# Kernel optimization log

Hardware: AMD Instinct MI355X
Metric: run time of the kernel (lower is better)

## Reference

```python
import jax, jax.numpy as jnp
import numpy as np

TOP_K = 2  # num_expert in the torch module


def setup_inputs() -> dict:
    key = jax.random.key(0)
    ks = jax.random.split(key, 8)
    B, C, H, W, E, Dh = 8, 512, 32, 32, 8, 1024
    inputs = jax.random.normal(ks[0], (B, C, H, W), dtype=jnp.float32)
    k = jax.random.uniform(ks[1], (B, 1, 1, 1), dtype=jnp.float32)
    # gate: global-avg-pool + Linear(C -> E)
    Wg = jax.random.normal(ks[2], (C, E), dtype=jnp.float32) / np.sqrt(C)
    bg = jnp.zeros((E,), dtype=jnp.float32)
    # experts: per-expert 2-layer channel MLP (1x1-conv style), modulated by k
    W1 = jax.random.normal(ks[3], (E, C, Dh), dtype=jnp.float32) / np.sqrt(C)
    b1 = jnp.zeros((E, Dh), dtype=jnp.float32)
    W2 = jax.random.normal(ks[4], (E, Dh, C), dtype=jnp.float32) / np.sqrt(Dh)
    b2 = jnp.zeros((E, C), dtype=jnp.float32)
    return {"inputs": inputs, "k": k, "Wg": Wg, "bg": bg,
            "W1": W1, "b1": b1, "W2": W2, "b2": b2}


def reference(inputs, k, Wg, bg, W1, b1, W2, b2):
    B = inputs.shape[0]
    # --- gate: softmax in fp32, cast back (matches F.softmax(dtype=torch.float)) ---
    logits = jnp.mean(inputs, axis=(2, 3)) @ Wg + bg            # [B, E]
    weights = jax.nn.softmax(logits.astype(jnp.float32), axis=1).astype(inputs.dtype)
    topk_w, topk_idx = jax.lax.top_k(weights, TOP_K)            # [B, K]
    # --- scatter top-k gate weights into dense [B, E] mask (training path) ---
    exp_w = jnp.zeros_like(weights).at[jnp.arange(B)[:, None], topk_idx].set(topk_w)
    # --- run ALL experts densely (training-mode math), masked combine ---
    h = jnp.einsum('bchw,ecd->bedhw', inputs, W1) + b1[None, :, :, None, None]
    h = jax.nn.gelu(h, approximate=False)                        # [B,E,Dh,H,W]
    y = jnp.einsum('bedhw,edc->bechw', h, W2) + b2[None, :, :, None, None]
    y = y * k[:, None]                                           # per-sample scalar mod
    out = inputs + jnp.einsum('bechw,be->bchw', y, exp_w)        # residual + weighted sum
    return out
```

## Files before the change

### kernel.cpp

```cpp
#include <hip/hip_runtime.h>
#include <hip/hip_bf16.h>
#include <math.h>


typedef __bf16 bf16_t;
typedef __attribute__((ext_vector_type(8))) __bf16 bf16x8;
typedef __attribute__((ext_vector_type(4))) __bf16 bf16x4;
typedef __attribute__((ext_vector_type(4))) float f32x4;

#define GLDS(g, l) __builtin_amdgcn_global_load_lds(                      \
    (const __attribute__((address_space(1))) void*)(const void*)(g),       \
    (__attribute__((address_space(3))) void*)(void*)(l), 16, 0, 0)

__device__ __forceinline__ int xcd_swz(int bid, int grid) {
    return (bid & 7) * (grid >> 3) + (bid >> 3);
}

__device__ __forceinline__ float gelu_fast(float x) {
    float z = x * 0.70710678118654752f;
    float az = fabsf(z);
    float t = 1.0f / (1.0f + 0.3275911f * az);
    float p = ((((1.061405429f * t - 1.453152027f) * t + 1.421413741f) * t
                - 0.284496736f) * t + 0.254829592f) * t;
    float e = __expf(-az * az);
    float er = copysignf(1.0f - p * e, z);
    return 0.5f * x * (1.0f + er);
}

__global__ __launch_bounds__(256) void transpose_cvt_all(
    const float* __restrict__ x, const float* __restrict__ W1,
    const float* __restrict__ W2, bf16_t* __restrict__ xT,
    bf16_t* __restrict__ W1t, bf16_t* __restrict__ W2t, float* __restrict__ pp) {
    int id = blockIdx.x;
    const float* src; bf16_t* dst; int Rows, Cols, csh; bool dm = false;
    if (id < 1024)      { src = x;  dst = xT;  Rows = 512;  Cols = 1024; csh = 4; dm = true; }
    else if (id < 2048) { id -= 1024; src = W1; dst = W1t; Rows = 512;  Cols = 1024; csh = 4; }
    else                { id -= 2048; src = W2; dst = W2t; Rows = 1024; Cols = 512; csh = 3; }
    const int bz = id >> 7, t = id & 127;
    const int ct = t & ((1 << csh) - 1), rt = t >> csh;
    const int r0 = rt * 64, c0 = ct * 64;
    __shared__ float tile[64][65];
    const int tid = threadIdx.x;
    const int lrw = tid >> 4, lcol = (tid & 15) * 4;
    const float* sb = src + (size_t)bz * Rows * Cols + c0;
    #pragma unroll
    for (int p = 0; p < 4; ++p) {
        const int row = p * 16 + lrw;
        float4 v = *(const float4*)(sb + (size_t)(r0 + row) * Cols + lcol);
        tile[row][lcol + 0] = v.x; tile[row][lcol + 1] = v.y;
        tile[row][lcol + 2] = v.z; tile[row][lcol + 3] = v.w;
    }
    __syncthreads();
    if (dm) {
        const int row = tid >> 2, q = tid & 3;
        float s = 0.f;
        #pragma unroll
        for (int j = 0; j < 16; ++j) s += tile[row][q * 16 + j];
        s += __shfl_down(s, 2, 4);
        s += __shfl_down(s, 1, 4);
        if (q == 0) pp[(bz * 16 + ct) * 512 + r0 + row] = s;
    }
    bf16_t* db = dst + (size_t)bz * Rows * Cols + r0;
    #pragma unroll
    for (int q = 0; q < 2; ++q) {
        const int idq = q * 256 + tid;
        const int orow = idq >> 3, seg = idq & 7;
        bf16_t ov[8];
        #pragma unroll
        for (int j = 0; j < 8; ++j) ov[j] = (bf16_t)tile[seg * 8 + j][orow];
        *(bf16x8*)(db + (size_t)(c0 + orow) * Rows + seg * 8) = *(bf16x8*)ov;
    }
}

__global__ void gate_kernel(const float* __restrict__ pp, const float* __restrict__ Wg,
                            const float* __restrict__ bg, const float* __restrict__ kmod,
                            int* __restrict__ tidx, float* __restrict__ scale) {
    const int b = blockIdx.x;
    const int tid = threadIdx.x;
    const int lane = tid & 63, wave = tid >> 6;
    float a[8] = {0.f, 0.f, 0.f, 0.f, 0.f, 0.f, 0.f, 0.f};
    #pragma unroll
    for (int rep = 0; rep < 2; ++rep) {
        const int c = rep * 256 + tid;
        float m = 0.f;
        #pragma unroll
        for (int ht = 0; ht < 16; ++ht) m += pp[(b * 16 + ht) * 512 + c];
        #pragma unroll
        for (int e = 0; e < 8; ++e) a[e] += m * Wg[c * 8 + e];
    }
    #pragma unroll
    for (int e = 0; e < 8; ++e)
        #pragma unroll
        for (int off = 32; off; off >>= 1) a[e] += __shfl_xor(a[e], off, 64);
    __shared__ float red[4][8];
    if (lane == 0) {
        #pragma unroll
        for (int e = 0; e < 8; ++e) red[wave][e] = a[e];
    }
    __syncthreads();
    if (tid == 0) {
        float lg[8], mx = -1e30f;
        #pragma unroll
        for (int e = 0; e < 8; ++e) {
            lg[e] = (red[0][e] + red[1][e] + red[2][e] + red[3][e]) * (1.0f / 1024.0f) + bg[e];
            mx = fmaxf(mx, lg[e]);
        }
        float sum = 0.f;
        #pragma unroll
        for (int e = 0; e < 8; ++e) { lg[e] = expf(lg[e] - mx); sum += lg[e]; }
        float inv = 1.0f / sum;
        float best = -1.f; int i0 = 0;
        for (int j = 0; j < 8; ++j) { float w = lg[j] * inv; if (w > best) { best = w; i0 = j; } }
        float best2 = -1.f; int i1 = 0;
        for (int j = 0; j < 8; ++j) { if (j == i0) continue; float w = lg[j] * inv; if (w > best2) { best2 = w; i1 = j; } }
        float kb = kmod[b];
        tidx[b * 2] = i0; tidx[b * 2 + 1] = i1;
        scale[b * 2] = best * kb; scale[b * 2 + 1] = best2 * kb;
    }
}

__global__ __launch_bounds__(256, 2) void gemm1_kernel(
    const bf16_t* __restrict__ W1t, const bf16_t* __restrict__ xT,
    const float* __restrict__ b1, const int* __restrict__ tidx,
    const float* __restrict__ scale, bf16_t* __restrict__ hT) {
    __shared__ bf16_t smem[32768];
    const int bid = xcd_swz(blockIdx.x, 1024);
    const int pair = bid >> 6, rem = bid & 63;
    const int b = pair >> 1, slot = pair & 1;
    const int e = tidx[pair];
    const float s = scale[pair];
    const int d0 = (rem >> 3) * 128, n0 = (rem & 7) * 128;
    const int tid = threadIdx.x;
    const int lane = tid & 63, wave = tid >> 6;
    const int wm = (wave & 1) * 64, wn = (wave >> 1) * 64;
    const int lrow = lane & 15, quad = lane >> 4;

    const bf16_t* gA = W1t + (size_t)e * 524288 + (size_t)d0 * 512;
    const bf16_t* gB = xT + (size_t)b * 524288 + (size_t)n0 * 512;

    f32x4 acc[4][4];
    #pragma unroll
    for (int i = 0; i < 4; ++i)
        #pragma unroll
        for (int j = 0; j < 4; ++j) acc[i][j] = (f32x4){0.f, 0.f, 0.f, 0.f};

    auto stage = [&](int st, int it) {
        const int k0 = it * 64;
        bf16_t* dst = smem + st * 16384;
        #pragma unroll
        for (int p = 0; p < 4; ++p) {
            const int row = p * 32 + (tid >> 3);
            const int cg = ((tid & 7) ^ (row & 7)) * 8;
            GLDS(gA + (size_t)row * 512 + k0 + cg, dst + (p * 256 + tid) * 8);
            GLDS(gB + (size_t)row * 512 + k0 + cg, dst + 8192 + (p * 256 + tid) * 8);
        }
    };

    stage(0, 0);
    stage(1, 1);

    for (int it = 0; it < 8; ++it) {
        const int cur = it & 1;
        if (it < 7) {
            asm volatile("s_waitcnt vmcnt(8)" ::: "memory");
        } else {
            asm volatile("s_waitcnt vmcnt(0)" ::: "memory");
        }
        __builtin_amdgcn_s_barrier();
        const bf16_t* cA = smem + cur * 16384;
        const bf16_t* cB = cA + 8192;
        #pragma unroll
        for (int kh = 0; kh < 2; ++kh) {
            const int swz = ((kh * 4 + quad) ^ (lrow & 7)) * 8;
            bf16x8 af[4], bfr[4];
            #pragma unroll
            for (int i = 0; i < 4; ++i) {
                af[i]  = *(const bf16x8*)&cA[(wm + i * 16 + lrow) * 64 + swz];
                bfr[i] = *(const bf16x8*)&cB[(wn + i * 16 + lrow) * 64 + swz];
            }
            #pragma unroll
            for (int i = 0; i < 4; ++i)
                #pragma unroll
                for (int j = 0; j < 4; ++j)
                    acc[i][j] = __builtin_amdgcn_mfma_f32_16x16x32_bf16(af[i], bfr[j], acc[i][j], 0, 0, 0);
        }
        __builtin_amdgcn_s_barrier();
        if (it < 6) stage(cur, it + 2);
    }

    bf16_t* hTb = hT + (size_t)b * 2097152 + slot * 1024;
    #pragma unroll
    for (int i = 0; i < 4; ++i) {
        const int d_l = wm + i * 16 + quad * 4;
        const float4 bb = *(const float4*)(b1 + e * 1024 + d0 + d_l);
        #pragma unroll
        for (int j = 0; j < 4; ++j) {
            const int hw_l = wn + j * 16 + lrow;
            f32x4 a = acc[i][j];
            bf16x4 o = { (bf16_t)(gelu_fast(a[0] + bb.x) * s),
                         (bf16_t)(gelu_fast(a[1] + bb.y) * s),
                         (bf16_t)(gelu_fast(a[2] + bb.z) * s),
                         (bf16_t)(gelu_fast(a[3] + bb.w) * s) };
            *(bf16x4*)&smem[hw_l * 136 + d_l] = o;
        }
    }
    __syncthreads();
    #pragma unroll
    for (int q = 0; q < 8; ++q) {
        const int idx = q * 256 + tid;
        const int row = idx >> 4, c16 = idx & 15;
        bf16x8 v = *(const bf16x8*)&smem[row * 136 + c16 * 8];
        *(bf16x8*)(hTb + (size_t)(n0 + row) * 2048 + d0 + c16 * 8) = v;
    }
}

__global__ __launch_bounds__(256, 2) void gemm2_kernel(
    const bf16_t* __restrict__ W2t, const bf16_t* __restrict__ hT,
    const float* __restrict__ b2, const int* __restrict__ tidx,
    const float* __restrict__ scale, const float* __restrict__ x,
    float* __restrict__ out) {
    __shared__ bf16_t smem[24576];
    const int bid = xcd_swz(blockIdx.x, 512);
    const int b = bid >> 6, rem = bid & 63;
    const int c0 = (rem >> 3) * 64, hw0 = (rem & 7) * 128;
    const int e0 = tidx[b * 2], e1 = tidx[b * 2 + 1];
    const float s0 = scale[b * 2], s1 = scale[b * 2 + 1];
    const int tid = threadIdx.x;
    const int lane = tid & 63, wave = tid >> 6;
    const int wm = (wave & 1) * 64;
    const int wc = (wave >> 1) * 32;
    const int lrow = lane & 15, quad = lane >> 4;

    const bf16_t* hTb = hT + (size_t)b * 2097152 + (size_t)hw0 * 2048;
    const bf16_t* B0 = W2t + (size_t)e0 * 524288 + (size_t)c0 * 1024;
    const bf16_t* B1 = W2t + (size_t)e1 * 524288 + (size_t)c0 * 1024;

    float4 xr[2][4];
    #pragma unroll
    for (int j = 0; j < 2; ++j) {
        const int c = c0 + wc + j * 16 + lrow;
        #pragma unroll
        for (int i = 0; i < 4; ++i) {
            const int hw = hw0 + wm + i * 16 + quad * 4;
            xr[j][i] = *(const float4*)(x + ((size_t)(b * 512 + c)) * 1024 + hw);
        }
    }

    f32x4 acc[4][2];
    #pragma unroll
    for (int i = 0; i < 4; ++i)
        #pragma unroll
        for (int j = 0; j < 2; ++j) acc[i][j] = (f32x4){0.f, 0.f, 0.f, 0.f};

    auto stage = [&](int st, int it) {
        const int k0 = it * 64;
        bf16_t* dst = smem + st * 12288;
        #pragma unroll
        for (int p = 0; p < 4; ++p) {
            const int row = p * 32 + (tid >> 3);
            const int cg = ((tid & 7) ^ (row & 7)) * 8;
            GLDS(hTb + (size_t)row * 2048 + k0 + cg, dst + (p * 256 + tid) * 8);
        }
        const bf16_t* gB = ((it < 16) ? B0 : B1) + (k0 & 1023);
        #pragma unroll
        for (int p = 0; p < 2; ++p) {
            const int row = p * 32 + (tid >> 3);
            const int cg = ((tid & 7) ^ (row & 7)) * 8;
            GLDS(gB + (size_t)row * 1024 + cg, dst + 8192 + (p * 256 + tid) * 8);
        }
    };

    stage(0, 0);
    stage(1, 1);

    for (int it = 0; it < 32; ++it) {
        const int cur = it & 1;
        if (it < 31) {
            asm volatile("s_waitcnt vmcnt(6)" ::: "memory");
        } else {
            asm volatile("s_waitcnt vmcnt(0)" ::: "memory");
        }
        __builtin_amdgcn_s_barrier();
        const bf16_t* cA = smem + cur * 12288;
        const bf16_t* cB = cA + 8192;
        #pragma unroll
        for (int kh = 0; kh < 2; ++kh) {
            const int swz = ((kh * 4 + quad) ^ (lrow & 7)) * 8;
            bf16x8 af[4], bfr[2];
            #pragma unroll
            for (int i = 0; i < 4; ++i)
                af[i] = *(const bf16x8*)&cA[(wm + i * 16 + lrow) * 64 + swz];
            #pragma unroll
            for (int j = 0; j < 2; ++j)
                bfr[j] = *(const bf16x8*)&cB[(wc + j * 16 + lrow) * 64 + swz];
            #pragma unroll
            for (int i = 0; i < 4; ++i)
                #pragma unroll
                for (int j = 0; j < 2; ++j)
                    acc[i][j] = __builtin_amdgcn_mfma_f32_16x16x32_bf16(af[i], bfr[j], acc[i][j], 0, 0, 0);
        }
        __builtin_amdgcn_s_barrier();
        if (it < 30) stage(cur, it + 2);
    }

    #pragma unroll
    for (int j = 0; j < 2; ++j) {
        const int c = c0 + wc + j * 16 + lrow;
        const float bias = s0 * b2[e0 * 512 + c] + s1 * b2[e1 * 512 + c];
        #pragma unroll
        for (int i = 0; i < 4; ++i) {
            const int hw = hw0 + wm + i * 16 + quad * 4;
            const size_t o = ((size_t)(b * 512 + c)) * 1024 + hw;
            const float4 xv = xr[j][i];
            float4 ov = { acc[i][j][0] + xv.x + bias, acc[i][j][1] + xv.y + bias,
                          acc[i][j][2] + xv.z + bias, acc[i][j][3] + xv.w + bias };
            *(float4*)(out + o) = ov;
        }
    }
}

extern "C" void kernel_launch(void* const* d_in, const int* in_sizes, int n_in,
                              void* d_out, int out_size, void* d_ws, size_t ws_size,
                              hipStream_t stream) {
    const float* x    = (const float*)d_in[0];
    const float* kmod = (const float*)d_in[1];
    const float* Wg   = (const float*)d_in[2];
    const float* bg   = (const float*)d_in[3];
    const float* W1   = (const float*)d_in[4];
    const float* b1   = (const float*)d_in[5];
    const float* W2   = (const float*)d_in[6];
    const float* b2   = (const float*)d_in[7];
    float* out = (float*)d_out;

    char* ws = (char*)d_ws;
    int*   tix  = (int*)ws;
    float* scl  = (float*)(ws + 64);
    bf16_t* xT  = (bf16_t*)(ws + 32768);
    bf16_t* W1t = (bf16_t*)(ws + 32768 + (size_t)8388608);
    bf16_t* W2t = (bf16_t*)(ws + 32768 + (size_t)2 * 8388608);
    bf16_t* hT  = (bf16_t*)(ws + 32768 + (size_t)3 * 8388608);
    float* pp   = (float*)hT;

    transpose_cvt_all<<<3072, 256, 0, stream>>>(x, W1, W2, xT, W1t, W2t, pp);
    gate_kernel<<<8, 256, 0, stream>>>(pp, Wg, bg, kmod, tix, scl);
    gemm1_kernel<<<1024, 256, 0, stream>>>(W1t, xT, b1, tix, scl, hT);
    gemm2_kernel<<<512, 256, 0, stream>>>(W2t, hT, b2, tix, scl, x, out);
}
```

Measured before the change: 162.7 us.

## Fuse gate into gemm1 prologue and triple-buffer gemm2 pipeline

Removes the separate gate kernel launch: each gemm1 block now recomputes the gate softmax and top-2 for its sample from the pooled partial sums, and one block per sample writes the indices and scales that gemm2 reads. The pooled partial sums move to their own workspace region so gemm1 no longer overwrites them while writing hT. gemm2 goes from a 2-stage to a 3-stage LDS pipeline with adjusted vmcnt waits, to hide more global-load latency. The cost is redundant gate work in all 1024 gemm1 blocks plus two extra barriers in each, and larger LDS use in gemm2 that could reduce occupancy.

```diff
diff --git a/kernel.cpp b/kernel.cpp
--- a/kernel.cpp
+++ b/kernel.cpp
@@ -72,68 +72,73 @@
     }
 }
 
-__global__ void gate_kernel(const float* __restrict__ pp, const float* __restrict__ Wg,
-                            const float* __restrict__ bg, const float* __restrict__ kmod,
-                            int* __restrict__ tidx, float* __restrict__ scale) {
-    const int b = blockIdx.x;
-    const int tid = threadIdx.x;
-    const int lane = tid & 63, wave = tid >> 6;
-    float a[8] = {0.f, 0.f, 0.f, 0.f, 0.f, 0.f, 0.f, 0.f};
-    #pragma unroll
-    for (int rep = 0; rep < 2; ++rep) {
-        const int c = rep * 256 + tid;
-        float m = 0.f;
-        #pragma unroll
-        for (int ht = 0; ht < 16; ++ht) m += pp[(b * 16 + ht) * 512 + c];
-        #pragma unroll
-        for (int e = 0; e < 8; ++e) a[e] += m * Wg[c * 8 + e];
-    }
-    #pragma unroll
-    for (int e = 0; e < 8; ++e)
-        #pragma unroll
-        for (int off = 32; off; off >>= 1) a[e] += __shfl_xor(a[e], off, 64);
-    __shared__ float red[4][8];
-    if (lane == 0) {
-        #pragma unroll
-        for (int e = 0; e < 8; ++e) red[wave][e] = a[e];
-    }
-    __syncthreads();
-    if (tid == 0) {
-        float lg[8], mx = -1e30f;
-        #pragma unroll
-        for (int e = 0; e < 8; ++e) {
-            lg[e] = (red[0][e] + red[1][e] + red[2][e] + red[3][e]) * (1.0f / 1024.0f) + bg[e];
-            mx = fmaxf(mx, lg[e]);
-        }
-        float sum = 0.f;
-        #pragma unroll
-        for (int e = 0; e < 8; ++e) { lg[e] = expf(lg[e] - mx); sum += lg[e]; }
-        float inv = 1.0f / sum;
-        float best = -1.f; int i0 = 0;
-        for (int j = 0; j < 8; ++j) { float w = lg[j] * inv; if (w > best) { best = w; i0 = j; } }
-        float best2 = -1.f; int i1 = 0;
-        for (int j = 0; j < 8; ++j) { if (j == i0) continue; float w = lg[j] * inv; if (w > best2) { best2 = w; i1 = j; } }
-        float kb = kmod[b];
-        tidx[b * 2] = i0; tidx[b * 2 + 1] = i1;
-        scale[b * 2] = best * kb; scale[b * 2 + 1] = best2 * kb;
-    }
-}
-
 __global__ __launch_bounds__(256, 2) void gemm1_kernel(
     const bf16_t* __restrict__ W1t, const bf16_t* __restrict__ xT,
-    const float* __restrict__ b1, const int* __restrict__ tidx,
-    const float* __restrict__ scale, bf16_t* __restrict__ hT) {
+    const float* __restrict__ b1, const float* __restrict__ pp,
+    const float* __restrict__ Wg, const float* __restrict__ bg,
+    const float* __restrict__ kmod, int* __restrict__ tidx,
+    float* __restrict__ scale, bf16_t* __restrict__ hT) {
     __shared__ bf16_t smem[32768];
+    __shared__ float gred[4][8];
+    __shared__ int   gsel_sh;
+    __shared__ float gscl_sh;
     const int bid = xcd_swz(blockIdx.x, 1024);
     const int pair = bid >> 6, rem = bid & 63;
     const int b = pair >> 1, slot = pair & 1;
-    const int e = tidx[pair];
-    const float s = scale[pair];
     const int d0 = (rem >> 3) * 128, n0 = (rem & 7) * 128;
     const int tid = threadIdx.x;
     const int lane = tid & 63, wave = tid >> 6;
     const int wm = (wave & 1) * 64, wn = (wave >> 1) * 64;
     const int lrow = lane & 15, quad = lane >> 4;
+
+    {
+        float a[8] = {0.f, 0.f, 0.f, 0.f, 0.f, 0.f, 0.f, 0.f};
+        #pragma unroll
+        for (int rep = 0; rep < 2; ++rep) {
+            const int c = rep * 256 + tid;
+            float m = 0.f;
+            #pragma unroll
+            for (int ht = 0; ht < 16; ++ht) m += pp[(b * 16 + ht) * 512 + c];
+            #pragma unroll
+            for (int e8 = 0; e8 < 8; ++e8) a[e8] += m * Wg[c * 8 + e8];
+        }
+        #pragma unroll
+        for (int e8 = 0; e8 < 8; ++e8)
+            #pragma unroll
+            for (int off = 32; off; off >>= 1) a[e8] += __shfl_xor(a[e8], off, 64);
+        if (lane == 0) {
+            #pragma unroll
+            for (int e8 = 0; e8 < 8; ++e8) gred[wave][e8] = a[e8];
+        }
+        __syncthreads();
+        if (tid == 0) {
+            float lg[8], mx = -1e30f;
+            #pragma unroll
+            for (int e8 = 0; e8 < 8; ++e8) {
+                lg[e8] = (gred[0][e8] + gred[1][e8] + gred[2][e8] + gred[3][e8])
+                         * (1.0f / 1024.0f) + bg[e8];
+                mx = fmaxf(mx, lg[e8]);
+            }
+            float sum = 0.f;
+            #pragma unroll
+            for (int e8 = 0; e8 < 8; ++e8) { lg[e8] = expf(lg[e8] - mx); sum += lg[e8]; }
+            float inv = 1.0f / sum;
+            float best = -1.f; int i0 = 0;
+            for (int j = 0; j < 8; ++j) { float w = lg[j] * inv; if (w > best) { best = w; i0 = j; } }
+            float best2 = -1.f; int i1 = 0;
+            for (int j = 0; j < 8; ++j) { if (j == i0) continue; float w = lg[j] * inv; if (w > best2) { best2 = w; i1 = j; } }
+            float kb = kmod[b];
+            gsel_sh = slot ? i1 : i0;
+            gscl_sh = (slot ? best2 : best) * kb;
+            if (rem == 0 && slot == 0) {
+                tidx[b * 2] = i0; tidx[b * 2 + 1] = i1;
+                scale[b * 2] = best * kb; scale[b * 2 + 1] = best2 * kb;
+            }
+        }
+        __syncthreads();
+    }
+    const int e = gsel_sh;
+    const float s = gscl_sh;
 
     const bf16_t* gA = W1t + (size_t)e * 524288 + (size_t)d0 * 512;
     const bf16_t* gB = xT + (size_t)b * 524288 + (size_t)n0 * 512;
@@ -219,7 +224,7 @@
     const float* __restrict__ b2, const int* __restrict__ tidx,
     const float* __restrict__ scale, const float* __restrict__ x,
     float* __restrict__ out) {
-    __shared__ bf16_t smem[24576];
+    __shared__ bf16_t smem[36864];
     const int bid = xcd_swz(blockIdx.x, 512);
     const int b = bid >> 6, rem = bid & 63;
     const int c0 = (rem >> 3) * 64, hw0 = (rem & 7) * 128;
@@ -272,10 +277,13 @@
 
     stage(0, 0);
     stage(1, 1);
-
+    stage(2, 2);
+
+    int cur = 0;
     for (int it = 0; it < 32; ++it) {
-        const int cur = it & 1;
-        if (it < 31) {
+        if (it <= 29) {
+            asm volatile("s_waitcnt vmcnt(12)" ::: "memory");
+        } else if (it == 30) {
             asm volatile("s_waitcnt vmcnt(6)" ::: "memory");
         } else {
             asm volatile("s_waitcnt vmcnt(0)" ::: "memory");
@@ -300,7 +308,8 @@
                     acc[i][j] = __builtin_amdgcn_mfma_f32_16x16x32_bf16(af[i], bfr[j], acc[i][j], 0, 0, 0);
         }
         __builtin_amdgcn_s_barrier();
-        if (it < 30) stage(cur, it + 2);
+        if (it <= 28) stage(cur, it + 3);
+        cur = (cur == 2) ? 0 : cur + 1;
     }
 
     #pragma unroll
@@ -339,10 +348,9 @@
     bf16_t* W1t = (bf16_t*)(ws + 32768 + (size_t)8388608);
     bf16_t* W2t = (bf16_t*)(ws + 32768 + (size_t)2 * 8388608);
     bf16_t* hT  = (bf16_t*)(ws + 32768 + (size_t)3 * 8388608);
-    float* pp   = (float*)hT;
+    float* pp   = (float*)(ws + 32768 + (size_t)3 * 8388608 + (size_t)33554432);
 
     transpose_cvt_all<<<3072, 256, 0, stream>>>(x, W1, W2, xT, W1t, W2t, pp);
-    gate_kernel<<<8, 256, 0, stream>>>(pp, Wg, bg, kmod, tix, scl);
-    gemm1_kernel<<<1024, 256, 0, stream>>>(W1t, xT, b1, tix, scl, hT);
+    gemm1_kernel<<<1024, 256, 0, stream>>>(W1t, xT, b1, pp, Wg, bg, kmod, tix, scl, hT);
     gemm2_kernel<<<512, 256, 0, stream>>>(W2t, hT, b2, tix, scl, x, out);
 }
```

Result: slower. 167.2 us (+2.8%).
